# Performance work log

Hardware: AMD Instinct MI355X
Metric: run time of the kernel (lower is better)

The kernel has to match this reference:

```python
import jax, jax.numpy as jnp
import numpy as np

N_EMBED = 384
N_HEADS = 6
HEAD_SIZE = 64


def setup_inputs() -> dict:
    key = jax.random.key(0)
    ks = jax.random.split(key, 6)
    B, T = 16, 1024
    x = jax.random.normal(ks[0], (B, T, N_EMBED), dtype=jnp.float32)
    s = 1.0 / np.sqrt(N_EMBED)
    wq = jax.random.normal(ks[1], (N_HEADS, N_EMBED, HEAD_SIZE), dtype=jnp.float32) * s
    wk = jax.random.normal(ks[2], (N_HEADS, N_EMBED, HEAD_SIZE), dtype=jnp.float32) * s
    wv = jax.random.normal(ks[3], (N_HEADS, N_EMBED, HEAD_SIZE), dtype=jnp.float32) * s
    wp = jax.random.normal(ks[4], (N_EMBED, N_EMBED), dtype=jnp.float32) * s
    bp = jnp.zeros((N_EMBED,), dtype=jnp.float32)
    return {"x": x, "wq": wq, "wk": wk, "wv": wv, "wp": wp, "bp": bp}


def reference(x, wq, wk, wv, wp, bp):
    B, T, C = x.shape
    # per-head projections: [B,H,T,D]
    q = jnp.einsum('btc,hcd->bhtd', x, wq)
    k = jnp.einsum('btc,hcd->bhtd', x, wk)
    v = jnp.einsum('btc,hcd->bhtd', x, wv)
    # NOTE: original scales by 1/sqrt(C) with C = embed dim (384), no causal mask
    scores = jnp.einsum('bhtd,bhsd->bhts', q, k) / jnp.sqrt(jnp.asarray(C, x.dtype))
    weights = jax.nn.softmax(scores, axis=-1)  # dropout = identity (eval)
    out = jnp.einsum('bhts,bhsd->bhtd', weights, v)
    # concat heads -> [B,T,H*D]
    out = out.transpose(0, 2, 1, 3).reshape(B, T, -1)
    return out @ wp.T + bp
```

## Files before the change

kernel.cpp:

```cpp
#include <hip/hip_runtime.h>
#include <hip/hip_bf16.h>

#define Hn 6
#define Tn 1024
#define Cn 384
#define Dn 64
#define Bn 16
#define Mn (Bn*Tn)
#define QSCALE 0.07362222f

typedef __attribute__((ext_vector_type(8)))  short s16x8;
typedef __attribute__((ext_vector_type(16))) float f32x16;

__device__ __forceinline__ void gl_lds16(const void* g, void* l) {
  __builtin_amdgcn_global_load_lds(
      (const __attribute__((address_space(1))) unsigned int*)g,
      (__attribute__((address_space(3))) unsigned int*)l, 16, 0, 0);
}
__device__ __forceinline__ unsigned pk2f(float a, float b) {
  __hip_bfloat162 h = __float22bfloat162_rn(make_float2(a, b));
  union { __hip_bfloat162 h; unsigned u; } cv; cv.h = h; return cv.u;
}
__device__ __forceinline__ f32x16 mfma32(s16x8 a, s16x8 b, f32x16 c) {
  return __builtin_amdgcn_mfma_f32_32x32x16_bf16(a, b, c, 0, 0, 0);
}

__global__ __launch_bounds__(256) void convert_all(
    const float* __restrict__ x, const float* __restrict__ wq,
    const float* __restrict__ wk, const float* __restrict__ wv,
    const float* __restrict__ wp,
    __hip_bfloat16* __restrict__ xb, __hip_bfloat16* __restrict__ wt,
    __hip_bfloat16* __restrict__ wpb)
{
  const int bid = blockIdx.x, t = threadIdx.x;
  if (bid < 18) {
    __shared__ float lt[64][65];
    const int mat = bid / Hn, hh = bid % Hn;
    const float* src = (mat == 0 ? wq : mat == 1 ? wk : wv) + (size_t)hh * (Cn*Dn);
    __hip_bfloat16* dst = wt + (size_t)mat * (Hn*Dn*Cn) + (size_t)hh * (Dn*Cn);
    const float sc = (mat == 0) ? QSCALE : 1.0f;
    for (int ct = 0; ct < 6; ++ct) {
      __syncthreads();
      #pragma unroll
      for (int ps = 0; ps < 4; ++ps) {
        int idx = ps*256 + t;
        int cl = idx >> 4, s4 = idx & 15;
        float4 v = *reinterpret_cast<const float4*>(src + (size_t)(ct*64 + cl)*Dn + s4*4);
        lt[cl][s4*4+0] = v.x * sc; lt[cl][s4*4+1] = v.y * sc;
        lt[cl][s4*4+2] = v.z * sc; lt[cl][s4*4+3] = v.w * sc;
      }
      __syncthreads();
      const int dd = t >> 2, cq = t & 3;
      #pragma unroll
      for (int i = 0; i < 16; ++i)
        dst[(size_t)dd*Cn + ct*64 + cq*16 + i] = __float2bfloat16(lt[cq*16 + i][dd]);
    }
  } else if (bid < 90) {
    const size_t base = (size_t)(bid - 18) * 2048 + (size_t)t * 8;
    float4 a = *reinterpret_cast<const float4*>(wp + base);
    float4 b = *reinterpret_cast<const float4*>(wp + base + 4);
    uint4 r; r.x = pk2f(a.x,a.y); r.y = pk2f(a.z,a.w); r.z = pk2f(b.x,b.y); r.w = pk2f(b.z,b.w);
    *reinterpret_cast<uint4*>((char*)wpb + base*2) = r;
  } else {
    const size_t base = (size_t)(bid - 90) * 2048 + (size_t)t * 8;
    float4 a = *reinterpret_cast<const float4*>(x + base);
    float4 b = *reinterpret_cast<const float4*>(x + base + 4);
    uint4 r; r.x = pk2f(a.x,a.y); r.y = pk2f(a.z,a.w); r.z = pk2f(b.x,b.y); r.w = pk2f(b.z,b.w);
    *reinterpret_cast<uint4*>((char*)xb + base*2) = r;
  }
}

__global__ __launch_bounds__(256) void qkv_proj(
    const __hip_bfloat16* __restrict__ xb, const __hip_bfloat16* __restrict__ wt,
    __hip_bfloat16* __restrict__ qo, __hip_bfloat16* __restrict__ ko,
    __hip_bfloat16* __restrict__ vto)
{
  __shared__ __align__(16) char sm[32768];
  const int t = threadIdx.x, lane = t & 63, w = t >> 6;
  const int hi = lane >> 5, nl = lane & 31;
  const int wr = w >> 1, wc = w & 1;
  const int m0 = blockIdx.x * 64;
  const int mat = blockIdx.y / Hn, h = blockIdx.y % Hn;
  const __hip_bfloat16* wb = wt + (size_t)mat*(Hn*Dn*Cn) + (size_t)h*(Dn*Cn);

  const int mrow = wr*32 + nl;
  const int nrow = wc*32 + nl;
  f32x16 acc = {};

  auto stage = [&](int bb, int s) {
    #pragma unroll
    for (int c = 0; c < 4; ++c) {
      const int off = w*4096 + c*1024 + lane*16;
      const char* src;
      if (off < 8192) {
        const int row = off >> 7, sl = (off >> 4) & 7;
        src = (const char*)xb + (size_t)(m0 + row)*768 + s*128 + ((sl ^ (row & 7)) * 16);
      } else {
        const int o2 = off - 8192;
        const int row = o2 >> 7, sl = (o2 >> 4) & 7;
        src = (const char*)wb + (size_t)row*768 + s*128 + ((sl ^ (row & 7)) * 16);
      }
      gl_lds16(src, sm + bb + w*4096 + c*1024);
    }
  };
  auto compute = [&](int bb) {
    __builtin_amdgcn_s_setprio(1);
    #pragma unroll
    for (int kk = 0; kk < 4; ++kk) {
      s16x8 a  = *reinterpret_cast<const s16x8*>(sm + bb + mrow*128 + (((2*kk + hi) ^ (mrow & 7)) * 16));
      s16x8 bv = *reinterpret_cast<const s16x8*>(sm + bb + 8192 + nrow*128 + (((2*kk + hi) ^ (nrow & 7)) * 16));
      acc = mfma32(a, bv, acc);
    }
    __builtin_amdgcn_s_setprio(0);
  };

  stage(0, 0);
  __syncthreads();
  for (int s = 0; s < 6; s += 2) {
    stage(16384, s + 1);
    compute(0);
    __syncthreads();
    if (s + 2 < 6) stage(0, s + 2);
    compute(16384);
    __syncthreads();
  }

  const int d = wc*32 + nl;
  if (mat < 2) {
    __hip_bfloat16* op = (mat == 0) ? qo : ko;
    #pragma unroll
    for (int r = 0; r < 16; ++r) {
      const int ml = wr*32 + (r & 3) + 8*(r >> 2) + 4*hi;
      const int M = m0 + ml, bI = M >> 10, tl = M & 1023;
      op[(((size_t)bI*Hn + h)*Tn + tl)*Dn + d] = __float2bfloat16(acc[r]);
    }
  } else {
    #pragma unroll
    for (int rq = 0; rq < 4; ++rq) {
      const int ml = wr*32 + 8*rq + 4*hi;
      const int M = m0 + ml, bI = M >> 10, tl = M & 1023;
      const unsigned u0 = pk2f(acc[rq*4+0], acc[rq*4+1]);
      const unsigned u1 = pk2f(acc[rq*4+2], acc[rq*4+3]);
      const unsigned long long v = ((unsigned long long)u1 << 32) | u0;
      *reinterpret_cast<unsigned long long*>(
          (char*)vto + ((((size_t)bI*Hn + h)*Dn + d)*Tn + tl)*2) = v;
    }
  }
}

__global__ __launch_bounds__(256) void attn_fwd(
    const __hip_bfloat16* __restrict__ qb, const __hip_bfloat16* __restrict__ kb,
    const __hip_bfloat16* __restrict__ vtb, __hip_bfloat16* __restrict__ ao)
{
  __shared__ __align__(16) char smem[32768];
  const int t = threadIdx.x, lane = t & 63, w = t >> 6;
  const int hi = lane >> 5, qm = lane & 31;
  const int l7 = lane & 7;
  const int bx = blockIdx.x;
  const int bh = bx % 96, qt = bx / 96;
  const int b = bh / Hn, h = bh % Hn;

  const int qrow = qt*128 + w*32 + qm;
  const __hip_bfloat16* qrp = qb + ((size_t)bh*Tn + qrow)*Dn;
  s16x8 qf[4];
  #pragma unroll
  for (int hh = 0; hh < 4; ++hh)
    qf[hh] = *reinterpret_cast<const s16x8*>(qrp + hh*16 + hi*8);

  const size_t kbase = (size_t)bh * Tn * Dn;
  const size_t vbase = (size_t)bh * Dn * Tn;

  f32x16 oacc[2] = {};
  float lsum = 0.f;

  auto stage = [&](int bb, int kt) {
    #pragma unroll
    for (int c = 0; c < 4; ++c) {
      const int off = w*4096 + c*1024 + lane*16;
      const char* src;
      if (off < 8192) {
        const int row = off >> 7, sl = (off >> 4) & 7;
        src = (const char*)(kb + kbase + (size_t)(kt*64 + row)*Dn) + ((sl ^ (row & 7)) * 16);
      } else {
        const int o2 = off - 8192;
        const int row = o2 >> 7, sl = (o2 >> 4) & 7;
        src = (const char*)(vtb + vbase + (size_t)row*Tn + kt*64) + ((sl ^ (row & 7)) * 16);
      }
      gl_lds16(src, smem + bb + w*4096 + c*1024);
    }
  };

  auto compute = [&](int bb) {
    f32x16 sacc[2] = {};
    __builtin_amdgcn_s_setprio(1);
    #pragma unroll
    for (int ts = 0; ts < 2; ++ts) {
      const int srow = ts*32 + qm;
      #pragma unroll
      for (int hh = 0; hh < 4; ++hh) {
        s16x8 ka = *reinterpret_cast<const s16x8*>(
            smem + bb + srow*128 + (((2*hh + hi) ^ l7) * 16));
        sacc[ts] = mfma32(ka, qf[hh], sacc[ts]);
      }
    }
    __builtin_amdgcn_s_setprio(0);
    #pragma unroll
    for (int ts = 0; ts < 2; ++ts)
      #pragma unroll
      for (int r = 0; r < 16; ++r) { float p = exp2f(sacc[ts][r]); sacc[ts][r] = p; lsum += p; }

    #pragma unroll
    for (int m = 0; m < 4; ++m) {
      const int ts = m >> 1, rb = 8*(m & 1);
      const unsigned A0 = pk2f(sacc[ts][rb+0], sacc[ts][rb+1]);
      const unsigned A1 = pk2f(sacc[ts][rb+2], sacc[ts][rb+3]);
      const unsigned B0 = pk2f(sacc[ts][rb+4], sacc[ts][rb+5]);
      const unsigned B1 = pk2f(sacc[ts][rb+6], sacc[ts][rb+7]);
      const unsigned s0 = hi ? A0 : B0;
      const unsigned s1 = hi ? A1 : B1;
      const unsigned r0 = __shfl_xor(s0, 32);
      const unsigned r1 = __shfl_xor(s1, 32);
      union { unsigned u[4]; s16x8 v; } fr;
      fr.u[0] = hi ? r0 : A0;  fr.u[1] = hi ? r1 : A1;
      fr.u[2] = hi ? B0 : r0;  fr.u[3] = hi ? B1 : r1;
      __builtin_amdgcn_s_setprio(1);
      #pragma unroll
      for (int dt = 0; dt < 2; ++dt) {
        const int drow = dt*32 + qm;
        s16x8 va = *reinterpret_cast<const s16x8*>(
            smem + bb + 8192 + drow*128 + (((2*m + hi) ^ l7) * 16));
        oacc[dt] = mfma32(va, fr.v, oacc[dt]);
      }
      __builtin_amdgcn_s_setprio(0);
    }
  };

  stage(0, 0);
  __syncthreads();
  for (int kt = 0; kt < 16; kt += 2) {
    stage(16384, kt + 1);
    compute(0);
    __syncthreads();
    if (kt + 2 < 16) stage(0, kt + 2);
    compute(16384);
    __syncthreads();
  }

  lsum += __shfl_xor(lsum, 32);
  const float inv = 1.0f / lsum;

  const int qloc = w*32 + qm;
  #pragma unroll
  for (int dt = 0; dt < 2; ++dt)
    #pragma unroll
    for (int rq = 0; rq < 4; ++rq) {
      const unsigned u0 = pk2f(oacc[dt][rq*4+0]*inv, oacc[dt][rq*4+1]*inv);
      const unsigned u1 = pk2f(oacc[dt][rq*4+2]*inv, oacc[dt][rq*4+3]*inv);
      const unsigned long long v = ((unsigned long long)u1 << 32) | u0;
      *reinterpret_cast<unsigned long long*>(
          smem + qloc*128 + (((4*dt + rq) ^ (qm & 7)) * 16) + 8*hi) = v;
    }
  __syncthreads();
  {
    const int qr = t >> 1, half = t & 1;
    char* dst = (char*)ao + ((size_t)(b*Tn + qt*128 + qr))*(Cn*2) + (h*Dn + half*32)*2;
    #pragma unroll
    for (int sl = 0; sl < 4; ++sl) {
      uint4 v = *reinterpret_cast<const uint4*>(
          smem + qr*128 + (((half*4 + sl) ^ (qr & 7)) * 16));
      *reinterpret_cast<uint4*>(dst + sl*16) = v;
    }
  }
}

__global__ __launch_bounds__(256) void out_proj(
    const __hip_bfloat16* __restrict__ ab, const __hip_bfloat16* __restrict__ wpb,
    const float* __restrict__ bp, float* __restrict__ out)
{
  __shared__ __align__(16) char sm[32768];
  const int t = threadIdx.x, lane = t & 63, w = t >> 6;
  const int hi = lane >> 5, nl = lane & 31;
  const int wr = w >> 1, wc = w & 1;
  const int m0 = blockIdx.x * 64;
  const int n0 = blockIdx.y * 64;

  const int mrow = wr*32 + nl;
  const int nrow = wc*32 + nl;
  f32x16 acc = {};

  auto stage = [&](int bb, int s) {
    #pragma unroll
    for (int c = 0; c < 4; ++c) {
      const int off = w*4096 + c*1024 + lane*16;
      const char* src;
      if (off < 8192) {
        const int row = off >> 7, sl = (off >> 4) & 7;
        src = (const char*)ab + (size_t)(m0 + row)*768 + s*128 + ((sl ^ (row & 7)) * 16);
      } else {
        const int o2 = off - 8192;
        const int row = o2 >> 7, sl = (o2 >> 4) & 7;
        src = (const char*)wpb + (size_t)(n0 + row)*768 + s*128 + ((sl ^ (row & 7)) * 16);
      }
      gl_lds16(src, sm + bb + w*4096 + c*1024);
    }
  };
  auto compute = [&](int bb) {
    __builtin_amdgcn_s_setprio(1);
    #pragma unroll
    for (int kk = 0; kk < 4; ++kk) {
      s16x8 a  = *reinterpret_cast<const s16x8*>(sm + bb + mrow*128 + (((2*kk + hi) ^ (mrow & 7)) * 16));
      s16x8 bv = *reinterpret_cast<const s16x8*>(sm + bb + 8192 + nrow*128 + (((2*kk + hi) ^ (nrow & 7)) * 16));
      acc = mfma32(a, bv, acc);
    }
    __builtin_amdgcn_s_setprio(0);
  };

  stage(0, 0);
  __syncthreads();
  for (int s = 0; s < 6; s += 2) {
    stage(16384, s + 1);
    compute(0);
    __syncthreads();
    if (s + 2 < 6) stage(0, s + 2);
    compute(16384);
    __syncthreads();
  }

  const int n = n0 + wc*32 + nl;
  const float bv = bp[n];
  #pragma unroll
  for (int r = 0; r < 16; ++r) {
    const int ml = wr*32 + (r & 3) + 8*(r >> 2) + 4*hi;
    out[(size_t)(m0 + ml)*Cn + n] = acc[r] + bv;
  }
}

extern "C" void kernel_launch(void* const* d_in, const int* in_sizes, int n_in,
                              void* d_out, int out_size, void* d_ws, size_t ws_size,
                              hipStream_t stream) {
  const float* x  = (const float*)d_in[0];
  const float* wq = (const float*)d_in[1];
  const float* wk = (const float*)d_in[2];
  const float* wv = (const float*)d_in[3];
  const float* wp = (const float*)d_in[4];
  const float* bp = (const float*)d_in[5];
  float* out = (float*)d_out;

  unsigned char* W = (unsigned char*)d_ws;
  __hip_bfloat16* xb  = (__hip_bfloat16*)(W);
  __hip_bfloat16* wt  = (__hip_bfloat16*)(W + 12582912);
  __hip_bfloat16* wpb = (__hip_bfloat16*)(W + 13467648);
  __hip_bfloat16* qv  = (__hip_bfloat16*)(W + 13762560);
  __hip_bfloat16* kv  = (__hip_bfloat16*)(W + 26345472);
  __hip_bfloat16* vt  = (__hip_bfloat16*)(W + 38928384);
  __hip_bfloat16* at  = (__hip_bfloat16*)(W + 51511296);

  convert_all<<<3162, 256, 0, stream>>>(x, wq, wk, wv, wp, xb, wt, wpb);
  qkv_proj<<<dim3(Mn/64, 3*Hn), 256, 0, stream>>>(xb, wt, qv, kv, vt);
  attn_fwd<<<Bn*Hn*(Tn/128), 256, 0, stream>>>(qv, kv, vt, at);
  out_proj<<<dim3(Mn/64, Cn/64), 256, 0, stream>>>(at, wpb, bp, out);
}
```

Measured before the change: 183.5 us.

## Fuse x fp32-to-bf16 conversion into QKV projection and reuse x tile across heads

Removes the separate conversion pass that wrote a bf16 copy of x. The QKV projection now loads its 64-row fp32 x tile once, converts it into LDS with a swizzle, and keeps it resident while looping over all six heads. Only the weight tiles are double-buffered from global, and the grid shrinks from 18 to 3 blocks in y. In exchange each block uses 64KB of LDS, which lowers occupancy, and the grid has fewer blocks (768), which may underfill the GPU.

```diff
diff --git a/kernel.cpp b/kernel.cpp
--- a/kernel.cpp
+++ b/kernel.cpp
@@ -25,12 +25,10 @@
   return __builtin_amdgcn_mfma_f32_32x32x16_bf16(a, b, c, 0, 0, 0);
 }
 
-__global__ __launch_bounds__(256) void convert_all(
-    const float* __restrict__ x, const float* __restrict__ wq,
-    const float* __restrict__ wk, const float* __restrict__ wv,
-    const float* __restrict__ wp,
-    __hip_bfloat16* __restrict__ xb, __hip_bfloat16* __restrict__ wt,
-    __hip_bfloat16* __restrict__ wpb)
+__global__ __launch_bounds__(256) void convert_w(
+    const float* __restrict__ wq, const float* __restrict__ wk,
+    const float* __restrict__ wv, const float* __restrict__ wp,
+    __hip_bfloat16* __restrict__ wt, __hip_bfloat16* __restrict__ wpb)
 {
   const int bid = blockIdx.x, t = threadIdx.x;
   if (bid < 18) {
@@ -55,95 +53,101 @@
       for (int i = 0; i < 16; ++i)
         dst[(size_t)dd*Cn + ct*64 + cq*16 + i] = __float2bfloat16(lt[cq*16 + i][dd]);
     }
-  } else if (bid < 90) {
+  } else {
     const size_t base = (size_t)(bid - 18) * 2048 + (size_t)t * 8;
     float4 a = *reinterpret_cast<const float4*>(wp + base);
     float4 b = *reinterpret_cast<const float4*>(wp + base + 4);
     uint4 r; r.x = pk2f(a.x,a.y); r.y = pk2f(a.z,a.w); r.z = pk2f(b.x,b.y); r.w = pk2f(b.z,b.w);
     *reinterpret_cast<uint4*>((char*)wpb + base*2) = r;
-  } else {
-    const size_t base = (size_t)(bid - 90) * 2048 + (size_t)t * 8;
-    float4 a = *reinterpret_cast<const float4*>(x + base);
-    float4 b = *reinterpret_cast<const float4*>(x + base + 4);
-    uint4 r; r.x = pk2f(a.x,a.y); r.y = pk2f(a.z,a.w); r.z = pk2f(b.x,b.y); r.w = pk2f(b.z,b.w);
-    *reinterpret_cast<uint4*>((char*)xb + base*2) = r;
   }
 }
 
 __global__ __launch_bounds__(256) void qkv_proj(
-    const __hip_bfloat16* __restrict__ xb, const __hip_bfloat16* __restrict__ wt,
+    const float* __restrict__ x, const __hip_bfloat16* __restrict__ wt,
     __hip_bfloat16* __restrict__ qo, __hip_bfloat16* __restrict__ ko,
     __hip_bfloat16* __restrict__ vto)
 {
-  __shared__ __align__(16) char sm[32768];
+  __shared__ __align__(16) char sm[65536];
   const int t = threadIdx.x, lane = t & 63, w = t >> 6;
   const int hi = lane >> 5, nl = lane & 31;
   const int wr = w >> 1, wc = w & 1;
   const int m0 = blockIdx.x * 64;
-  const int mat = blockIdx.y / Hn, h = blockIdx.y % Hn;
-  const __hip_bfloat16* wb = wt + (size_t)mat*(Hn*Dn*Cn) + (size_t)h*(Dn*Cn);
+  const int mat = blockIdx.y;
+  const char* wbase = (const char*)(wt + (size_t)mat * (Hn*Dn*Cn));
 
   const int mrow = wr*32 + nl;
   const int nrow = wc*32 + nl;
+
+  auto stageW = [&](int h, int s, int buf) {
+    const char* wtile = wbase + (size_t)h * (Dn*Cn*2);
+    #pragma unroll
+    for (int r = 0; r < 2; ++r) {
+      const int off = w*2048 + r*1024 + lane*16;
+      const int row = off >> 7, sl = (off >> 4) & 7;
+      const char* src = wtile + (size_t)row*768 + s*128 + ((sl ^ (row & 7)) * 16);
+      gl_lds16(src, sm + 49152 + buf*8192 + w*2048 + r*1024);
+    }
+  };
+
+  stageW(0, 0, 0);
+  #pragma unroll 4
+  for (int p = 0; p < 24; ++p) {
+    const int idx = p*256 + t;
+    const int row = idx / 96, c4 = idx % 96;
+    const float4 v = *reinterpret_cast<const float4*>(x + (size_t)(m0 + row)*Cn + c4*4);
+    const unsigned long long pr =
+        ((unsigned long long)pk2f(v.z, v.w) << 32) | pk2f(v.x, v.y);
+    const int slot = c4 >> 1;
+    const int swz  = (slot & ~7) | ((slot ^ row) & 7);
+    *reinterpret_cast<unsigned long long*>(sm + row*768 + swz*16 + (c4 & 1)*8) = pr;
+  }
+  __syncthreads();
+
   f32x16 acc = {};
-
-  auto stage = [&](int bb, int s) {
-    #pragma unroll
-    for (int c = 0; c < 4; ++c) {
-      const int off = w*4096 + c*1024 + lane*16;
-      const char* src;
-      if (off < 8192) {
-        const int row = off >> 7, sl = (off >> 4) & 7;
-        src = (const char*)xb + (size_t)(m0 + row)*768 + s*128 + ((sl ^ (row & 7)) * 16);
-      } else {
-        const int o2 = off - 8192;
-        const int row = o2 >> 7, sl = (o2 >> 4) & 7;
-        src = (const char*)wb + (size_t)row*768 + s*128 + ((sl ^ (row & 7)) * 16);
-      }
-      gl_lds16(src, sm + bb + w*4096 + c*1024);
-    }
-  };
-  auto compute = [&](int bb) {
-    __builtin_amdgcn_s_setprio(1);
-    #pragma unroll
-    for (int kk = 0; kk < 4; ++kk) {
-      s16x8 a  = *reinterpret_cast<const s16x8*>(sm + bb + mrow*128 + (((2*kk + hi) ^ (mrow & 7)) * 16));
-      s16x8 bv = *reinterpret_cast<const s16x8*>(sm + bb + 8192 + nrow*128 + (((2*kk + hi) ^ (nrow & 7)) * 16));
-      acc = mfma32(a, bv, acc);
-    }
-    __builtin_amdgcn_s_setprio(0);
-  };
-
-  stage(0, 0);
-  __syncthreads();
-  for (int s = 0; s < 6; s += 2) {
-    stage(16384, s + 1);
-    compute(0);
-    __syncthreads();
-    if (s + 2 < 6) stage(0, s + 2);
-    compute(16384);
-    __syncthreads();
-  }
-
-  const int d = wc*32 + nl;
-  if (mat < 2) {
-    __hip_bfloat16* op = (mat == 0) ? qo : ko;
-    #pragma unroll
-    for (int r = 0; r < 16; ++r) {
-      const int ml = wr*32 + (r & 3) + 8*(r >> 2) + 4*hi;
-      const int M = m0 + ml, bI = M >> 10, tl = M & 1023;
-      op[(((size_t)bI*Hn + h)*Tn + tl)*Dn + d] = __float2bfloat16(acc[r]);
-    }
-  } else {
-    #pragma unroll
-    for (int rq = 0; rq < 4; ++rq) {
-      const int ml = wr*32 + 8*rq + 4*hi;
-      const int M = m0 + ml, bI = M >> 10, tl = M & 1023;
-      const unsigned u0 = pk2f(acc[rq*4+0], acc[rq*4+1]);
-      const unsigned u1 = pk2f(acc[rq*4+2], acc[rq*4+3]);
-      const unsigned long long v = ((unsigned long long)u1 << 32) | u0;
-      *reinterpret_cast<unsigned long long*>(
-          (char*)vto + ((((size_t)bI*Hn + h)*Dn + d)*Tn + tl)*2) = v;
+  for (int h = 0; h < Hn; ++h) {
+    #pragma unroll
+    for (int s = 0; s < 6; ++s) {
+      if (!(h == 5 && s == 5)) {
+        const int nh = (s < 5) ? h : h + 1;
+        const int ns = (s < 5) ? s + 1 : 0;
+        stageW(nh, ns, (s + 1) & 1);
+      }
+      const int buf = s & 1;
+      __builtin_amdgcn_s_setprio(1);
+      #pragma unroll
+      for (int kk = 0; kk < 4; ++kk) {
+        s16x8 a = *reinterpret_cast<const s16x8*>(
+            sm + mrow*768 + (s*8 + ((2*kk + hi) ^ (mrow & 7))) * 16);
+        s16x8 bv = *reinterpret_cast<const s16x8*>(
+            sm + 49152 + buf*8192 + nrow*128 + (((2*kk + hi) ^ (nrow & 7)) * 16));
+        acc = mfma32(a, bv, acc);
+      }
+      __builtin_amdgcn_s_setprio(0);
+      if (s == 5) {
+        const int d = wc*32 + nl;
+        if (mat < 2) {
+          __hip_bfloat16* op = (mat == 0) ? qo : ko;
+          #pragma unroll
+          for (int r = 0; r < 16; ++r) {
+            const int ml = wr*32 + (r & 3) + 8*(r >> 2) + 4*hi;
+            const int M = m0 + ml, bI = M >> 10, tl = M & 1023;
+            op[(((size_t)bI*Hn + h)*Tn + tl)*Dn + d] = __float2bfloat16(acc[r]);
+          }
+        } else {
+          #pragma unroll
+          for (int rq = 0; rq < 4; ++rq) {
+            const int ml = wr*32 + 8*rq + 4*hi;
+            const int M = m0 + ml, bI = M >> 10, tl = M & 1023;
+            const unsigned u0 = pk2f(acc[rq*4+0], acc[rq*4+1]);
+            const unsigned u1 = pk2f(acc[rq*4+2], acc[rq*4+3]);
+            const unsigned long long v = ((unsigned long long)u1 << 32) | u0;
+            *reinterpret_cast<unsigned long long*>(
+                (char*)vto + ((((size_t)bI*Hn + h)*Dn + d)*Tn + tl)*2) = v;
+          }
+        }
+        acc = {};
+      }
+      __syncthreads();
     }
   }
 }
@@ -347,16 +351,15 @@
   float* out = (float*)d_out;
 
   unsigned char* W = (unsigned char*)d_ws;
-  __hip_bfloat16* xb  = (__hip_bfloat16*)(W);
-  __hip_bfloat16* wt  = (__hip_bfloat16*)(W + 12582912);
-  __hip_bfloat16* wpb = (__hip_bfloat16*)(W + 13467648);
-  __hip_bfloat16* qv  = (__hip_bfloat16*)(W + 13762560);
-  __hip_bfloat16* kv  = (__hip_bfloat16*)(W + 26345472);
-  __hip_bfloat16* vt  = (__hip_bfloat16*)(W + 38928384);
-  __hip_bfloat16* at  = (__hip_bfloat16*)(W + 51511296);
-
-  convert_all<<<3162, 256, 0, stream>>>(x, wq, wk, wv, wp, xb, wt, wpb);
-  qkv_proj<<<dim3(Mn/64, 3*Hn), 256, 0, stream>>>(xb, wt, qv, kv, vt);
+  __hip_bfloat16* wt  = (__hip_bfloat16*)(W);
+  __hip_bfloat16* wpb = (__hip_bfloat16*)(W + 884736);
+  __hip_bfloat16* qv  = (__hip_bfloat16*)(W + 1179648);
+  __hip_bfloat16* kv  = (__hip_bfloat16*)(W + 13762560);
+  __hip_bfloat16* vt  = (__hip_bfloat16*)(W + 26345472);
+  __hip_bfloat16* at  = (__hip_bfloat16*)(W + 38928384);
+
+  convert_w<<<90, 256, 0, stream>>>(wq, wk, wv, wp, wt, wpb);
+  qkv_proj<<<dim3(Mn/64, 3), 256, 0, stream>>>(x, wt, qv, kv, vt);
   attn_fwd<<<Bn*Hn*(Tn/128), 256, 0, stream>>>(qv, kv, vt, at);
   out_proj<<<dim3(Mn/64, Cn/64), 256, 0, stream>>>(at, wpb, bp, out);
 }
```

New measurement: 194.0 us. 1.06x slower.
